# Optimization experiments

Measured on AMD Instinct MI355X. Metric: run time of the kernel, lower is better.

The kernel has to match this reference:

```python
import jax, jax.numpy as jnp
import numpy as np

N_USER = 100000
N_ITEM = 50000
N_NODES = N_USER + N_ITEM
EMB = 64
NNZ = 4000000
BATCH = 4096
N_LAYERS = 3  # len(eval(args.layer_size)) with layer_size=[64,64,64]


def setup_inputs() -> dict:
    key = jax.random.key(0)
    k = jax.random.split(key, 8)
    adj_rows = jax.random.randint(k[0], (NNZ,), 0, N_NODES, dtype=jnp.int32)
    adj_cols = jax.random.randint(k[1], (NNZ,), 0, N_NODES, dtype=jnp.int32)
    adj_vals = jax.random.uniform(k[2], (NNZ,), dtype=jnp.float32)
    user_emb = jax.random.normal(k[3], (N_USER, EMB), dtype=jnp.float32)
    item_emb = jax.random.normal(k[4], (N_ITEM, EMB), dtype=jnp.float32)
    users = jax.random.randint(k[5], (BATCH,), 0, N_USER, dtype=jnp.int32)
    pos_items = jax.random.randint(k[6], (BATCH,), 0, N_ITEM, dtype=jnp.int32)
    neg_items = jax.random.randint(k[7], (BATCH,), 0, N_ITEM, dtype=jnp.int32)
    return {
        "adj_rows": adj_rows, "adj_cols": adj_cols, "adj_vals": adj_vals,
        "user_emb": user_emb, "item_emb": item_emb,
        "users": users, "pos_items": pos_items, "neg_items": neg_items,
    }


def _spmm(rows, cols, vals, x):
    # sparse [N,N] @ dense [N,D] via gather + segment-sum (COO)
    gathered = vals[:, None] * x[cols]          # [nnz, D]
    return jax.ops.segment_sum(gathered, rows, num_segments=N_NODES)


def reference(adj_rows, adj_cols, adj_vals, user_emb, item_emb,
              users, pos_items, neg_items):
    ego = jnp.concatenate([user_emb, item_emb], axis=0)  # [N, D]
    # Source quirk: ego_embeddings is never updated in the layer loop, so
    # every layer appends the same A_hat @ ego; mean over [ego] + L copies.
    prop = _spmm(adj_rows, adj_cols, adj_vals, ego)      # [N, D]
    light_out = (ego + N_LAYERS * prop) / (N_LAYERS + 1)
    u_g = light_out[:N_USER]
    i_g = light_out[N_USER:]
    out = jnp.stack([u_g[users], i_g[pos_items], i_g[neg_items]], axis=0)
    return out  # [3, BATCH, EMB]
```

## Files before the change

### kernel.cpp

```cpp
#include <hip/hip_runtime.h>

#define N_USER 100000
#define N_ITEM 50000
#define N_NODES 150000
#define EMB 64
#define NNZ 4000000
#define BATCH 4096
#define NSLOTS (3 * BATCH)
#define CAP 128

#define BM_OFF   0
#define CUR_OFF  19200
#define CT_OFF   68352
#define PROP_OFF 668416
#define BKT_OFF  3814144

__global__ void mark_kernel(const int* __restrict__ users,
                            const int* __restrict__ pos_items,
                            const int* __restrict__ neg_items,
                            unsigned int* __restrict__ bitmask,
                            int* __restrict__ ctab) {
    int t = blockIdx.x * blockDim.x + threadIdx.x;
    int k = t >> 12;
    int i = t & 4095;
    int node;
    if (k == 0)      node = users[i];
    else if (k == 1) node = N_USER + pos_items[i];
    else             node = N_USER + neg_items[i];
    atomicOr(bitmask + (node >> 5), 1u << (node & 31));
    atomicCAS(ctab + node, -1, t);
}

__global__ void scatter_kernel(const int* __restrict__ rows,
                               const int* __restrict__ cols,
                               const float* __restrict__ vals,
                               const unsigned int* __restrict__ bitmask,
                               const int* __restrict__ ctab,
                               unsigned int* __restrict__ cursor,
                               uint2* __restrict__ bucket) {
    int tid = blockIdx.x * blockDim.x + threadIdx.x;
    int row = rows[tid];
    int col = cols[tid];
    float val = vals[tid];
    unsigned int w = bitmask[row >> 5];
    if ((w >> (row & 31)) & 1) {
        int cid = ctab[row];
        unsigned int pos = atomicAdd(cursor + cid, 1u);
        if (pos < CAP)
            bucket[(size_t)cid * CAP + pos] =
                make_uint2((unsigned int)col, __float_as_uint(val));
    }
}

__global__ void accum_kernel(const unsigned int* __restrict__ cursor,
                             const uint2* __restrict__ bucket,
                             const float* __restrict__ user_emb,
                             const float* __restrict__ item_emb,
                             float* __restrict__ prop) {
    int t = blockIdx.x * blockDim.x + threadIdx.x;
    int wv = t >> 6;
    int lane = t & 63;
    unsigned int n = cursor[wv];
    if (n > CAP) n = CAP;
    const uint2* bkt = bucket + (size_t)wv * CAP;
    float acc = 0.0f;
    for (unsigned int base = 0; base < n; base += 8) {
        #pragma unroll
        for (int u = 0; u < 8; u++) {
            unsigned int e = base + (unsigned int)u;
            uint2 ev = bkt[e < n ? e : n - 1];
            int c = (int)ev.x;
            float v = __uint_as_float(ev.y);
            const float* x = (c < N_USER) ? user_emb + (size_t)c * EMB
                                          : item_emb + (size_t)(c - N_USER) * EMB;
            float xv = x[lane];
            acc += (e < n) ? v * xv : 0.0f;
        }
    }
    prop[(size_t)wv * EMB + lane] = acc;
}

__global__ void gather_kernel(const int* __restrict__ users,
                              const int* __restrict__ pos_items,
                              const int* __restrict__ neg_items,
                              const float* __restrict__ user_emb,
                              const float* __restrict__ item_emb,
                              const int* __restrict__ ctab,
                              const float* __restrict__ prop,
                              float* __restrict__ out) {
    int t = blockIdx.x * blockDim.x + threadIdx.x;
    int slot = t >> 4;
    int sub = t & 15;
    int k = slot >> 12;
    int i = slot & 4095;
    int node;
    if (k == 0)      node = users[i];
    else if (k == 1) node = N_USER + pos_items[i];
    else             node = N_USER + neg_items[i];
    const float4* ego = (const float4*)((node < N_USER)
                          ? user_emb + (size_t)node * EMB
                          : item_emb + (size_t)(node - N_USER) * EMB);
    float4 e = ego[sub];
    int cid = ctab[node];
    float4 p = ((const float4*)(prop + (size_t)cid * EMB))[sub];
    float4 o;
    o.x = (e.x + 3.0f * p.x) * 0.25f;
    o.y = (e.y + 3.0f * p.y) * 0.25f;
    o.z = (e.z + 3.0f * p.z) * 0.25f;
    o.w = (e.w + 3.0f * p.w) * 0.25f;
    ((float4*)out)[t] = o;
}

extern "C" void kernel_launch(void* const* d_in, const int* in_sizes, int n_in,
                              void* d_out, int out_size, void* d_ws, size_t ws_size,
                              hipStream_t stream) {
    const int*   adj_rows = (const int*)  d_in[0];
    const int*   adj_cols = (const int*)  d_in[1];
    const float* adj_vals = (const float*)d_in[2];
    const float* user_emb = (const float*)d_in[3];
    const float* item_emb = (const float*)d_in[4];
    const int*   users    = (const int*)  d_in[5];
    const int*   pos      = (const int*)  d_in[6];
    const int*   neg      = (const int*)  d_in[7];
    float* out = (float*)d_out;

    unsigned int* bitmask = (unsigned int*)((char*)d_ws + BM_OFF);
    unsigned int* cursor  = (unsigned int*)((char*)d_ws + CUR_OFF);
    int*          ctab    = (int*)         ((char*)d_ws + CT_OFF);
    float*        prop    = (float*)       ((char*)d_ws + PROP_OFF);
    uint2*        bucket  = (uint2*)       ((char*)d_ws + BKT_OFF);

    hipMemsetAsync((char*)d_ws + BM_OFF, 0, CT_OFF, stream);
    hipMemsetAsync((char*)d_ws + CT_OFF, 0xFF, N_NODES * 4, stream);

    mark_kernel<<<48, 256, 0, stream>>>(users, pos, neg, bitmask, ctab);

    scatter_kernel<<<15625, 256, 0, stream>>>(adj_rows, adj_cols, adj_vals,
                                              bitmask, ctab, cursor, bucket);

    accum_kernel<<<3072, 256, 0, stream>>>(cursor, bucket, user_emb, item_emb, prop);

    gather_kernel<<<768, 256, 0, stream>>>(users, pos, neg,
                                           user_emb, item_emb, ctab, prop, out);
}
```

Baseline: 171.5 us.

## Fuse gather into accum via per-node slot lists, vectorize scatter loads

Mark builds a linked list of output slots per unique node (head/next), so accum writes the final output rows directly and the separate gather kernel and prop buffer go away. Accum waves for non-leader slots exit early. Scatter now reads four edges per thread with nontemporal vector loads, and the two workspace memsets are merged into one zero fill by encoding ctab as cid+1. This cuts one launch and the prop round trip, but adds serial list walking within each wave.

```diff
diff --git a/kernel.cpp b/kernel.cpp
--- a/kernel.cpp
+++ b/kernel.cpp
@@ -9,17 +9,24 @@
 #define NSLOTS (3 * BATCH)
 #define CAP 128
 
-#define BM_OFF   0
-#define CUR_OFF  19200
-#define CT_OFF   68352
-#define PROP_OFF 668416
-#define BKT_OFF  3814144
+#define BM_OFF    0
+#define CUR_OFF   19200
+#define HEAD_OFF  68352
+#define NEXT_OFF  117504
+#define CT_OFF    166656
+#define ZERO_BYTES 766656
+#define BKT_OFF   768000
+
+typedef int   i32x4 __attribute__((ext_vector_type(4)));
+typedef float f32x4 __attribute__((ext_vector_type(4)));
 
 __global__ void mark_kernel(const int* __restrict__ users,
                             const int* __restrict__ pos_items,
                             const int* __restrict__ neg_items,
                             unsigned int* __restrict__ bitmask,
-                            int* __restrict__ ctab) {
+                            int* __restrict__ ctab,
+                            int* __restrict__ head,
+                            int* __restrict__ next) {
     int t = blockIdx.x * blockDim.x + threadIdx.x;
     int k = t >> 12;
     int i = t & 4095;
@@ -28,23 +35,19 @@
     else if (k == 1) node = N_USER + pos_items[i];
     else             node = N_USER + neg_items[i];
     atomicOr(bitmask + (node >> 5), 1u << (node & 31));
-    atomicCAS(ctab + node, -1, t);
+    int w = atomicCAS(ctab + node, 0, t + 1);
+    int cid = (w == 0) ? t : (w - 1);
+    next[t] = atomicExch(head + cid, t + 1);
 }
 
-__global__ void scatter_kernel(const int* __restrict__ rows,
-                               const int* __restrict__ cols,
-                               const float* __restrict__ vals,
-                               const unsigned int* __restrict__ bitmask,
-                               const int* __restrict__ ctab,
-                               unsigned int* __restrict__ cursor,
-                               uint2* __restrict__ bucket) {
-    int tid = blockIdx.x * blockDim.x + threadIdx.x;
-    int row = rows[tid];
-    int col = cols[tid];
-    float val = vals[tid];
+__device__ __forceinline__ void scatter_edge(int row, int col, float val,
+                                             const unsigned int* __restrict__ bitmask,
+                                             const int* __restrict__ ctab,
+                                             unsigned int* __restrict__ cursor,
+                                             uint2* __restrict__ bucket) {
     unsigned int w = bitmask[row >> 5];
     if ((w >> (row & 31)) & 1) {
-        int cid = ctab[row];
+        int cid = ctab[row] - 1;
         unsigned int pos = atomicAdd(cursor + cid, 1u);
         if (pos < CAP)
             bucket[(size_t)cid * CAP + pos] =
@@ -52,14 +55,38 @@
     }
 }
 
+__global__ void scatter_kernel(const i32x4* __restrict__ rows4,
+                               const i32x4* __restrict__ cols4,
+                               const f32x4* __restrict__ vals4,
+                               const unsigned int* __restrict__ bitmask,
+                               const int* __restrict__ ctab,
+                               unsigned int* __restrict__ cursor,
+                               uint2* __restrict__ bucket) {
+    int t = blockIdx.x * blockDim.x + threadIdx.x;
+    if (t >= NNZ / 4) return;
+    i32x4 r = __builtin_nontemporal_load(rows4 + t);
+    i32x4 c = __builtin_nontemporal_load(cols4 + t);
+    f32x4 v = __builtin_nontemporal_load(vals4 + t);
+    #pragma unroll
+    for (int j = 0; j < 4; j++)
+        scatter_edge(r[j], c[j], v[j], bitmask, ctab, cursor, bucket);
+}
+
 __global__ void accum_kernel(const unsigned int* __restrict__ cursor,
                              const uint2* __restrict__ bucket,
                              const float* __restrict__ user_emb,
                              const float* __restrict__ item_emb,
-                             float* __restrict__ prop) {
+                             const int* __restrict__ head,
+                             const int* __restrict__ next,
+                             const int* __restrict__ users,
+                             const int* __restrict__ pos_items,
+                             const int* __restrict__ neg_items,
+                             float* __restrict__ out) {
     int t = blockIdx.x * blockDim.x + threadIdx.x;
     int wv = t >> 6;
     int lane = t & 63;
+    int h = head[wv];
+    if (h == 0) return;
     unsigned int n = cursor[wv];
     if (n > CAP) n = CAP;
     const uint2* bkt = bucket + (size_t)wv * CAP;
@@ -77,38 +104,22 @@
             acc += (e < n) ? v * xv : 0.0f;
         }
     }
-    prop[(size_t)wv * EMB + lane] = acc;
-}
-
-__global__ void gather_kernel(const int* __restrict__ users,
-                              const int* __restrict__ pos_items,
-                              const int* __restrict__ neg_items,
-                              const float* __restrict__ user_emb,
-                              const float* __restrict__ item_emb,
-                              const int* __restrict__ ctab,
-                              const float* __restrict__ prop,
-                              float* __restrict__ out) {
-    int t = blockIdx.x * blockDim.x + threadIdx.x;
-    int slot = t >> 4;
-    int sub = t & 15;
-    int k = slot >> 12;
-    int i = slot & 4095;
-    int node;
-    if (k == 0)      node = users[i];
-    else if (k == 1) node = N_USER + pos_items[i];
-    else             node = N_USER + neg_items[i];
-    const float4* ego = (const float4*)((node < N_USER)
-                          ? user_emb + (size_t)node * EMB
-                          : item_emb + (size_t)(node - N_USER) * EMB);
-    float4 e = ego[sub];
-    int cid = ctab[node];
-    float4 p = ((const float4*)(prop + (size_t)cid * EMB))[sub];
-    float4 o;
-    o.x = (e.x + 3.0f * p.x) * 0.25f;
-    o.y = (e.y + 3.0f * p.y) * 0.25f;
-    o.z = (e.z + 3.0f * p.z) * 0.25f;
-    o.w = (e.w + 3.0f * p.w) * 0.25f;
-    ((float4*)out)[t] = o;
+    float p3 = 3.0f * acc;
+    int s = h - 1;
+    while (true) {
+        int k = s >> 12;
+        int i = s & 4095;
+        int node;
+        if (k == 0)      node = users[i];
+        else if (k == 1) node = N_USER + pos_items[i];
+        else             node = N_USER + neg_items[i];
+        const float* ego = (node < N_USER) ? user_emb + (size_t)node * EMB
+                                           : item_emb + (size_t)(node - N_USER) * EMB;
+        out[(size_t)s * EMB + lane] = (ego[lane] + p3) * 0.25f;
+        int nx = next[s];
+        if (nx == 0) break;
+        s = nx - 1;
+    }
 }
 
 extern "C" void kernel_launch(void* const* d_in, const int* in_sizes, int n_in,
@@ -126,20 +137,20 @@
 
     unsigned int* bitmask = (unsigned int*)((char*)d_ws + BM_OFF);
     unsigned int* cursor  = (unsigned int*)((char*)d_ws + CUR_OFF);
+    int*          head    = (int*)         ((char*)d_ws + HEAD_OFF);
+    int*          next    = (int*)         ((char*)d_ws + NEXT_OFF);
     int*          ctab    = (int*)         ((char*)d_ws + CT_OFF);
-    float*        prop    = (float*)       ((char*)d_ws + PROP_OFF);
     uint2*        bucket  = (uint2*)       ((char*)d_ws + BKT_OFF);
 
-    hipMemsetAsync((char*)d_ws + BM_OFF, 0, CT_OFF, stream);
-    hipMemsetAsync((char*)d_ws + CT_OFF, 0xFF, N_NODES * 4, stream);
+    hipMemsetAsync(d_ws, 0, ZERO_BYTES, stream);
 
-    mark_kernel<<<48, 256, 0, stream>>>(users, pos, neg, bitmask, ctab);
+    mark_kernel<<<48, 256, 0, stream>>>(users, pos, neg, bitmask, ctab, head, next);
 
-    scatter_kernel<<<15625, 256, 0, stream>>>(adj_rows, adj_cols, adj_vals,
-                                              bitmask, ctab, cursor, bucket);
+    scatter_kernel<<<3907, 256, 0, stream>>>((const i32x4*)adj_rows,
+                                             (const i32x4*)adj_cols,
+                                             (const f32x4*)adj_vals,
+                                             bitmask, ctab, cursor, bucket);
 
-    accum_kernel<<<3072, 256, 0, stream>>>(cursor, bucket, user_emb, item_emb, prop);
-
-    gather_kernel<<<768, 256, 0, stream>>>(users, pos, neg,
-                                           user_emb, item_emb, ctab, prop, out);
+    accum_kernel<<<3072, 256, 0, stream>>>(cursor, bucket, user_emb, item_emb,
+                                           head, next, users, pos, neg, out);
 }
```

After: 160.8 us (median of 2 runs). 1.07x faster.
